# Kernel optimization log

Hardware: AMD Instinct MI355X
Metric: run time of the kernel (lower is better)

Reference implementation:

```python
import jax, jax.numpy as jnp
import numpy as np

WINDOW = 10
STRIDES = 1
EPS = 1e-5


def setup_inputs() -> dict:
    key = jax.random.key(0)
    B, T, F = 128, 512, 40
    tensors = jax.random.normal(key, (B, T, F), dtype=jnp.float32)
    return {"tensors": tensors}


def reference(tensors):
    # tensors: [B, T, F]
    B, T, F = tensors.shape
    # window start positions, replicating the module's iter_list logic
    starts = np.arange(0, T - WINDOW + 1, STRIDES)
    if (T - WINDOW) not in starts:
        starts = np.append(starts, T - WINDOW)
    # [S, W] gather indices -> windowed view [B, S, W, F]
    idx = starts[:, None] + np.arange(WINDOW)[None, :]
    xw = tensors[:, idx, :]  # [B, S, W, F]

    mean = xw.mean(axis=2)  # [B, S, F] == K.mean over window axis
    # K.std: population std (ddof=0) over the window axis
    std = jnp.sqrt(((xw - mean[:, :, None, :]) ** 2).mean(axis=2))  # [B, S, F]
    # K.switch(is_nan(std), mean-mean, std): NaN std -> 0
    std = jnp.where(jnp.isnan(std), jnp.zeros_like(std), std) + EPS

    # E[x_i * x_j] over window for all feature pairs: [B, S, F, F]
    Exy = jnp.einsum('bswi,bswj->bsij', xw, xw) / WINDOW
    cov = Exy - mean[:, :, :, None] * mean[:, :, None, :]
    corr = cov / (std[:, :, :, None] * std[:, :, None, :])  # [B, S, F, F]

    # itertools.combinations(range(F), 2) order == upper-triangular row-major
    iu, ju = np.triu_indices(F, 1)
    return corr[:, :, iu, ju]  # [B, S, C] with C = F*(F-1)/2
```

## Files before the change

### kernel.cpp

```cpp
#include <hip/hip_runtime.h>

#define BB   128
#define TT   512
#define FF   40
#define WW   10
#define NS   503
#define NP   780
#define SC   64
#define NCHUNK 8
#define ROWS (SC + WW - 1)
#define NSLOT 4
#define EPSC 1e-5f

__global__ __launch_bounds__(256, 4) void ts_corr_roll2(const float* __restrict__ in,
                                                        float* __restrict__ out) {
    const int blk = blockIdx.x;
    const int b   = blk / NCHUNK;
    const int c   = blk - b * NCHUNK;
    const int s0  = (c == NCHUNK - 1) ? (NS - SC) : c * SC;
    const int tid = threadIdx.x;

    __shared__ float  xs[ROWS][FF];
    __shared__ float2 st[SC][FF];

    const float4* src4 = (const float4*)(in + ((size_t)b * TT + s0) * FF);
    float4* xs4 = (float4*)&xs[0][0];
    #pragma unroll
    for (int k = 0; k < 3; ++k) {
        const int i = tid + k * 256;
        if (i < ROWS * FF / 4) xs4[i] = src4[i];
    }
    __syncthreads();

    #pragma unroll
    for (int k = 0; k < 10; ++k) {
        const int cell = tid + k * 256;
        const int t = cell / FF;
        const int f = cell - t * FF;
        float sx = 0.f, sxx = 0.f;
        #pragma unroll
        for (int w = 0; w < WW; ++w) {
            const float x = xs[t + w][f];
            sx += x; sxx += x * x;
        }
        const float m = sx * 0.1f;
        const float v = fmaxf(sxx * 0.1f - m * m, 0.f);
        const float istd = 1.0f / (sqrtf(v) + EPSC);
        st[t][f] = make_float2(istd, m * istd);
    }

    int  pi[NSLOT], pj[NSLOT];
    bool act[NSLOT];
    float sxy[NSLOT], ph[NSLOT][WW];
    #pragma unroll
    for (int k = 0; k < NSLOT; ++k) {
        const int p = tid + k * 256;
        act[k] = (p < NP);
        const int pp = act[k] ? p : 0;
        int i = (int)((79.0f - sqrtf((float)(6241 - 8 * pp))) * 0.5f);
        while (i > 0 && i * (79 - i) / 2 > pp) --i;
        while ((i + 1) * (79 - (i + 1)) / 2 <= pp) ++i;
        pi[k] = i;
        pj[k] = pp - i * (79 - i) / 2 + i + 1;
        float s = 0.f;
        #pragma unroll
        for (int w = 0; w < WW; ++w) {
            const float pr = xs[w][pi[k]] * xs[w][pj[k]];
            ph[k][w] = pr;
            s += pr;
        }
        sxy[k] = s;
    }
    __syncthreads();

    float* dst0 = out + (size_t)(b * NS + s0) * NP;
    for (int t0 = 0; t0 < SC; t0 += WW) {
        #pragma unroll
        for (int u = 0; u < WW; ++u) {
            const int t = t0 + u;
            if (t >= SC) break;
            float* dst = dst0 + (size_t)t * NP;
            #pragma unroll
            for (int k = 0; k < NSLOT; ++k) {
                if (!act[k]) continue;
                const float2 si = st[t][pi[k]];
                const float2 sj = st[t][pj[k]];
                dst[tid + k * 256] = sxy[k] * 0.1f * si.x * sj.x - si.y * sj.y;
                if (t + 1 < SC) {
                    const float pn = xs[t + WW][pi[k]] * xs[t + WW][pj[k]];
                    sxy[k] += pn - ph[k][u];
                    ph[k][u] = pn;
                }
            }
        }
    }
}

extern "C" void kernel_launch(void* const* d_in, const int* in_sizes, int n_in,
                              void* d_out, int out_size, void* d_ws, size_t ws_size,
                              hipStream_t stream) {
    const float* in = (const float*)d_in[0];
    float* out = (float*)d_out;
    ts_corr_roll2<<<BB * NCHUNK, 256, 0, stream>>>(in, out);
}
```

Measured before the change: 51.07 us.

## Map each thread to a strip of four adjacent pairs with vectorized LDS reads

Reassigns work so each of 210 threads handles one row and four consecutive column indices, loading neighbor features and stats as float4 from shared memory. Per-window stats are also computed four features at a time. This reduces LDS traffic and index math per pair, but global stores become strided per instruction and fewer threads are active.

```diff
diff --git a/kernel.cpp b/kernel.cpp
--- a/kernel.cpp
+++ b/kernel.cpp
@@ -9,10 +9,10 @@
 #define SC   64
 #define NCHUNK 8
 #define ROWS (SC + WW - 1)
-#define NSLOT 4
+#define NSTRIP 210
 #define EPSC 1e-5f
 
-__global__ __launch_bounds__(256, 4) void ts_corr_roll2(const float* __restrict__ in,
+__global__ __launch_bounds__(256, 4) void ts_corr_strip(const float* __restrict__ in,
                                                         float* __restrict__ out) {
     const int blk = blockIdx.x;
     const int b   = blk / NCHUNK;
@@ -27,70 +27,88 @@
     float4* xs4 = (float4*)&xs[0][0];
     #pragma unroll
     for (int k = 0; k < 3; ++k) {
-        const int i = tid + k * 256;
-        if (i < ROWS * FF / 4) xs4[i] = src4[i];
+        const int idx = tid + k * 256;
+        if (idx < ROWS * FF / 4) xs4[idx] = src4[idx];
     }
     __syncthreads();
 
     #pragma unroll
-    for (int k = 0; k < 10; ++k) {
-        const int cell = tid + k * 256;
-        const int t = cell / FF;
-        const int f = cell - t * FF;
-        float sx = 0.f, sxx = 0.f;
-        #pragma unroll
-        for (int w = 0; w < WW; ++w) {
-            const float x = xs[t + w][f];
-            sx += x; sxx += x * x;
+    for (int k = 0; k < 3; ++k) {
+        const int qd = tid + k * 256;
+        if (qd < SC * FF / 4) {
+            const int t  = qd / 10;
+            const int f0 = (qd - t * 10) * 4;
+            float sx0=0,sx1=0,sx2=0,sx3=0, sq0=0,sq1=0,sq2=0,sq3=0;
+            #pragma unroll
+            for (int w = 0; w < WW; ++w) {
+                const float4 x = *(const float4*)&xs[t + w][f0];
+                sx0 += x.x; sx1 += x.y; sx2 += x.z; sx3 += x.w;
+                sq0 += x.x*x.x; sq1 += x.y*x.y; sq2 += x.z*x.z; sq3 += x.w*x.w;
+            }
+            const float m0 = sx0*0.1f, m1 = sx1*0.1f, m2 = sx2*0.1f, m3 = sx3*0.1f;
+            const float u0 = 1.f/(sqrtf(fmaxf(sq0*0.1f - m0*m0, 0.f)) + EPSC);
+            const float u1 = 1.f/(sqrtf(fmaxf(sq1*0.1f - m1*m1, 0.f)) + EPSC);
+            const float u2 = 1.f/(sqrtf(fmaxf(sq2*0.1f - m2*m2, 0.f)) + EPSC);
+            const float u3 = 1.f/(sqrtf(fmaxf(sq3*0.1f - m3*m3, 0.f)) + EPSC);
+            *(float4*)&st[t][f0]     = make_float4(u0, m0*u0, u1, m1*u1);
+            *(float4*)&st[t][f0 + 2] = make_float4(u2, m2*u2, u3, m3*u3);
         }
-        const float m = sx * 0.1f;
-        const float v = fmaxf(sxx * 0.1f - m * m, 0.f);
-        const float istd = 1.0f / (sqrtf(v) + EPSC);
-        st[t][f] = make_float2(istd, m * istd);
     }
 
-    int  pi[NSLOT], pj[NSLOT];
-    bool act[NSLOT];
-    float sxy[NSLOT], ph[NSLOT][WW];
+    int row = 0, j0 = 0;
+    const bool sact = (tid < NSTRIP);
+    {
+        int rem = sact ? tid : 0;
+        for (int r = 0; r < FF; ++r) {
+            const int cnt = 10 - ((r + 1) >> 2);
+            if (rem < cnt) { row = r; j0 = (((r + 1) >> 2) + rem) << 2; break; }
+            rem -= cnt;
+        }
+    }
+    bool val[4];
     #pragma unroll
-    for (int k = 0; k < NSLOT; ++k) {
-        const int p = tid + k * 256;
-        act[k] = (p < NP);
-        const int pp = act[k] ? p : 0;
-        int i = (int)((79.0f - sqrtf((float)(6241 - 8 * pp))) * 0.5f);
-        while (i > 0 && i * (79 - i) / 2 > pp) --i;
-        while ((i + 1) * (79 - (i + 1)) / 2 <= pp) ++i;
-        pi[k] = i;
-        pj[k] = pp - i * (79 - i) / 2 + i + 1;
-        float s = 0.f;
-        #pragma unroll
-        for (int w = 0; w < WW; ++w) {
-            const float pr = xs[w][pi[k]] * xs[w][pj[k]];
-            ph[k][w] = pr;
-            s += pr;
-        }
-        sxy[k] = s;
+    for (int q = 0; q < 4; ++q) val[q] = sact && (j0 + q > row);
+    const int rowoff = row * (79 - row) / 2 - row - 1;
+
+    float sxy[4] = {0.f, 0.f, 0.f, 0.f};
+    float ph[4][WW];
+    #pragma unroll
+    for (int w = 0; w < WW; ++w) {
+        const float  xi = xs[w][row];
+        const float4 xj = *(const float4*)&xs[w][j0];
+        const float p0 = xi*xj.x, p1 = xi*xj.y, p2 = xi*xj.z, p3 = xi*xj.w;
+        ph[0][w] = p0; sxy[0] += p0;
+        ph[1][w] = p1; sxy[1] += p1;
+        ph[2][w] = p2; sxy[2] += p2;
+        ph[3][w] = p3; sxy[3] += p3;
     }
     __syncthreads();
 
-    float* dst0 = out + (size_t)(b * NS + s0) * NP;
+    if (!sact) return;
+
+    float* dst0 = out + (size_t)(b * NS + s0) * NP + rowoff;
     for (int t0 = 0; t0 < SC; t0 += WW) {
         #pragma unroll
         for (int u = 0; u < WW; ++u) {
             const int t = t0 + u;
-            if (t >= SC) break;
+            if (t0 == 60 && u >= 4) break;
+            const float2 sti = st[t][row];
+            const float4 a0  = *(const float4*)&st[t][j0];
+            const float4 a1  = *(const float4*)&st[t][j0 + 2];
+            const float  sui = sti.x * 0.1f;
             float* dst = dst0 + (size_t)t * NP;
-            #pragma unroll
-            for (int k = 0; k < NSLOT; ++k) {
-                if (!act[k]) continue;
-                const float2 si = st[t][pi[k]];
-                const float2 sj = st[t][pj[k]];
-                dst[tid + k * 256] = sxy[k] * 0.1f * si.x * sj.x - si.y * sj.y;
-                if (t + 1 < SC) {
-                    const float pn = xs[t + WW][pi[k]] * xs[t + WW][pj[k]];
-                    sxy[k] += pn - ph[k][u];
-                    ph[k][u] = pn;
-                }
+            if (val[0]) dst[j0]     = sxy[0] * sui * a0.x - sti.y * a0.y;
+            if (val[1]) dst[j0 + 1] = sxy[1] * sui * a0.z - sti.y * a0.w;
+            if (val[2]) dst[j0 + 2] = sxy[2] * sui * a1.x - sti.y * a1.y;
+            if (val[3]) dst[j0 + 3] = sxy[3] * sui * a1.z - sti.y * a1.w;
+            if (t + 1 < SC) {
+                const float  xi = xs[t + WW][row];
+                const float4 xj = *(const float4*)&xs[t + WW][j0];
+                float pn;
+                pn = xi*xj.x; sxy[0] += pn - ph[0][u]; ph[0][u] = pn;
+                pn = xi*xj.y; sxy[1] += pn - ph[1][u]; ph[1][u] = pn;
+                pn = xi*xj.z; sxy[2] += pn - ph[2][u]; ph[2][u] = pn;
+                pn = xi*xj.w; sxy[3] += pn - ph[3][u]; ph[3][u] = pn;
             }
         }
     }
@@ -101,5 +119,5 @@
                               hipStream_t stream) {
     const float* in = (const float*)d_in[0];
     float* out = (float*)d_out;
-    ts_corr_roll2<<<BB * NCHUNK, 256, 0, stream>>>(in, out);
+    ts_corr_strip<<<BB * NCHUNK, 256, 0, stream>>>(in, out);
 }
```

After: 110.9 us. 117% more time.

## Vectorize stats pass, fold 1/W into scale, and unroll output loop two rows at a time

Applied to the files above, without the earlier changes.

The per-window mean and inverse-std pass now handles four features per thread with float4 shared loads and stores. The 0.1 factor is folded into the stored scale as sqrt(0.1), which drops one multiply per output. The output loop is hand-unrolled by two time steps, with shared loads batched ahead and the rolling sum update interleaved between them. Per-slot active checks are replaced by a tid<12 branch for the fourth slot. All of this aims to cut LDS and ALU instruction count in the output-bound loop, at the cost of more registers and a hard-coded schedule.

```diff
diff --git a/kernel.cpp b/kernel.cpp
--- a/kernel.cpp
+++ b/kernel.cpp
@@ -9,18 +9,18 @@
 #define SC   64
 #define NCHUNK 8
 #define ROWS (SC + WW - 1)
-#define NSLOT 4
 #define EPSC 1e-5f
+#define C01  0.31622776601683794f
 
-__global__ __launch_bounds__(256, 4) void ts_corr_roll2(const float* __restrict__ in,
-                                                        float* __restrict__ out) {
+__global__ __launch_bounds__(256, 4) void ts_corr_r6(const float* __restrict__ in,
+                                                     float* __restrict__ out) {
     const int blk = blockIdx.x;
     const int b   = blk / NCHUNK;
     const int c   = blk - b * NCHUNK;
     const int s0  = (c == NCHUNK - 1) ? (NS - SC) : c * SC;
     const int tid = threadIdx.x;
 
-    __shared__ float  xs[ROWS][FF];
+    __shared__ float  xs[SC + WW][FF];
     __shared__ float2 st[SC][FF];
 
     const float4* src4 = (const float4*)(in + ((size_t)b * TT + s0) * FF);
@@ -33,30 +33,34 @@
     __syncthreads();
 
     #pragma unroll
-    for (int k = 0; k < 10; ++k) {
-        const int cell = tid + k * 256;
-        const int t = cell / FF;
-        const int f = cell - t * FF;
-        float sx = 0.f, sxx = 0.f;
-        #pragma unroll
-        for (int w = 0; w < WW; ++w) {
-            const float x = xs[t + w][f];
-            sx += x; sxx += x * x;
+    for (int k = 0; k < 3; ++k) {
+        const int qd = tid + k * 256;
+        if (qd < SC * FF / 4) {
+            const int t  = qd / 10;
+            const int f0 = (qd - t * 10) * 4;
+            float sx0=0,sx1=0,sx2=0,sx3=0, sq0=0,sq1=0,sq2=0,sq3=0;
+            #pragma unroll
+            for (int w = 0; w < WW; ++w) {
+                const float4 x = *(const float4*)&xs[t + w][f0];
+                sx0 += x.x; sx1 += x.y; sx2 += x.z; sx3 += x.w;
+                sq0 += x.x*x.x; sq1 += x.y*x.y; sq2 += x.z*x.z; sq3 += x.w*x.w;
+            }
+            const float m0 = sx0*0.1f, m1 = sx1*0.1f, m2 = sx2*0.1f, m3 = sx3*0.1f;
+            const float u0 = 1.f/(sqrtf(fmaxf(sq0*0.1f - m0*m0, 0.f)) + EPSC);
+            const float u1 = 1.f/(sqrtf(fmaxf(sq1*0.1f - m1*m1, 0.f)) + EPSC);
+            const float u2 = 1.f/(sqrtf(fmaxf(sq2*0.1f - m2*m2, 0.f)) + EPSC);
+            const float u3 = 1.f/(sqrtf(fmaxf(sq3*0.1f - m3*m3, 0.f)) + EPSC);
+            *(float4*)&st[t][f0]     = make_float4(u0*C01, m0*u0, u1*C01, m1*u1);
+            *(float4*)&st[t][f0 + 2] = make_float4(u2*C01, m2*u2, u3*C01, m3*u3);
         }
-        const float m = sx * 0.1f;
-        const float v = fmaxf(sxx * 0.1f - m * m, 0.f);
-        const float istd = 1.0f / (sqrtf(v) + EPSC);
-        st[t][f] = make_float2(istd, m * istd);
     }
 
-    int  pi[NSLOT], pj[NSLOT];
-    bool act[NSLOT];
-    float sxy[NSLOT], ph[NSLOT][WW];
+    int pi[4], pj[4];
+    float sxy[4], ph[4][WW];
     #pragma unroll
-    for (int k = 0; k < NSLOT; ++k) {
+    for (int k = 0; k < 4; ++k) {
         const int p = tid + k * 256;
-        act[k] = (p < NP);
-        const int pp = act[k] ? p : 0;
+        const int pp = (p < NP) ? p : 0;
         int i = (int)((79.0f - sqrtf((float)(6241 - 8 * pp))) * 0.5f);
         while (i > 0 && i * (79 - i) / 2 > pp) --i;
         while ((i + 1) * (79 - (i + 1)) / 2 <= pp) ++i;
@@ -73,27 +77,55 @@
     }
     __syncthreads();
 
-    float* dst0 = out + (size_t)(b * NS + s0) * NP;
-    for (int t0 = 0; t0 < SC; t0 += WW) {
-        #pragma unroll
-        for (int u = 0; u < WW; ++u) {
-            const int t = t0 + u;
-            if (t >= SC) break;
-            float* dst = dst0 + (size_t)t * NP;
-            #pragma unroll
-            for (int k = 0; k < NSLOT; ++k) {
-                if (!act[k]) continue;
-                const float2 si = st[t][pi[k]];
-                const float2 sj = st[t][pj[k]];
-                dst[tid + k * 256] = sxy[k] * 0.1f * si.x * sj.x - si.y * sj.y;
-                if (t + 1 < SC) {
-                    const float pn = xs[t + WW][pi[k]] * xs[t + WW][pj[k]];
-                    sxy[k] += pn - ph[k][u];
-                    ph[k][u] = pn;
-                }
-            }
-        }
+    float* dst0 = out + (size_t)(b * NS + s0) * NP + tid;
+
+#define STEP2(U, TA, DO2) do {                                                  \
+    const int _tA = (TA);                                                       \
+    float* _dA = dst0 + (size_t)_tA * NP;                                       \
+    float* _dB = _dA + NP;                                                      \
+    _Pragma("unroll")                                                           \
+    for (int k = 0; k < 3; ++k) {                                               \
+        const int _ii = pi[k], _jj = pj[k];                                     \
+        const float  _xiA = xs[_tA + WW][_ii], _xiB = xs[_tA + WW + 1][_ii];    \
+        const float  _xjA = xs[_tA + WW][_jj], _xjB = xs[_tA + WW + 1][_jj];    \
+        const float2 _siA = st[_tA][_ii],      _siB = st[_tA + 1][_ii];         \
+        const float2 _sjA = st[_tA][_jj],      _sjB = st[_tA + 1][_jj];         \
+        _dA[k * 256] = sxy[k] * _siA.x * _sjA.x - _siA.y * _sjA.y;              \
+        const float _pn = _xiA * _xjA;                                          \
+        sxy[k] += _pn - ph[k][U]; ph[k][U] = _pn;                               \
+        _dB[k * 256] = sxy[k] * _siB.x * _sjB.x - _siB.y * _sjB.y;              \
+        if (DO2) {                                                              \
+            const float _p2 = _xiB * _xjB;                                      \
+            sxy[k] += _p2 - ph[k][(U) + 1]; ph[k][(U) + 1] = _p2;               \
+        }                                                                       \
+    }                                                                           \
+    if (tid < 12) {                                                             \
+        const int _ii = pi[3], _jj = pj[3];                                     \
+        const float  _xiA = xs[_tA + WW][_ii], _xiB = xs[_tA + WW + 1][_ii];    \
+        const float  _xjA = xs[_tA + WW][_jj], _xjB = xs[_tA + WW + 1][_jj];    \
+        const float2 _siA = st[_tA][_ii],      _siB = st[_tA + 1][_ii];         \
+        const float2 _sjA = st[_tA][_jj],      _sjB = st[_tA + 1][_jj];         \
+        _dA[768] = sxy[3] * _siA.x * _sjA.x - _siA.y * _sjA.y;                  \
+        const float _pn = _xiA * _xjA;                                          \
+        sxy[3] += _pn - ph[3][U]; ph[3][U] = _pn;                               \
+        _dB[768] = sxy[3] * _siB.x * _sjB.x - _siB.y * _sjB.y;                  \
+        if (DO2) {                                                              \
+            const float _p2 = _xiB * _xjB;                                      \
+            sxy[3] += _p2 - ph[3][(U) + 1]; ph[3][(U) + 1] = _p2;               \
+        }                                                                       \
+    }                                                                           \
+} while (0)
+
+    for (int t0 = 0; t0 < 60; t0 += WW) {
+        STEP2(0, t0,     true);
+        STEP2(2, t0 + 2, true);
+        STEP2(4, t0 + 4, true);
+        STEP2(6, t0 + 6, true);
+        STEP2(8, t0 + 8, true);
     }
+    STEP2(0, 60, true);
+    STEP2(2, 62, false);
+#undef STEP2
 }
 
 extern "C" void kernel_launch(void* const* d_in, const int* in_sizes, int n_in,
@@ -101,5 +133,5 @@
                               hipStream_t stream) {
     const float* in = (const float*)d_in[0];
     float* out = (float*)d_out;
-    ts_corr_roll2<<<BB * NCHUNK, 256, 0, stream>>>(in, out);
+    ts_corr_r6<<<BB * NCHUNK, 256, 0, stream>>>(in, out);
 }
```

Result: faster. 47.34 us (-7.3%).

## Transpose shared tiles, store stats as half2, use 512 threads with vectorized rolling updates

Applied to the files above, without the earlier changes.

Stores the input window transposed (feature-major) in shared memory so each thread can read four consecutive time steps of its pair features with single float4 loads, and stores the per-time inverse std and scaled mean as packed half2 values read four at a time. The mean/std pass becomes a rolling sliding-window update per feature instead of recomputing each window. Blocks grow to 512 threads with two pair slots per thread, and the time loop is manually unrolled in steps of four. The aim is to cut LDS instruction count and per-thread overhead in the store-bound inner loop. Keeping the statistics in fp16 lowers correlation precision and may exceed tolerance.

```diff
diff --git a/kernel.cpp b/kernel.cpp
--- a/kernel.cpp
+++ b/kernel.cpp
@@ -1,4 +1,5 @@
 #include <hip/hip_runtime.h>
+#include <hip/hip_fp16.h>
 
 #define BB   128
 #define TT   512
@@ -8,55 +9,68 @@
 #define NP   780
 #define SC   64
 #define NCHUNK 8
-#define ROWS (SC + WW - 1)
-#define NSLOT 4
+#define NT   512
+#define XCOL 76
+#define SCOL 68
 #define EPSC 1e-5f
+#define C01  0.31622776601683794f
 
-__global__ __launch_bounds__(256, 4) void ts_corr_roll2(const float* __restrict__ in,
-                                                        float* __restrict__ out) {
+__global__ __launch_bounds__(NT) void ts_corr_r14(const float* __restrict__ in,
+                                                  float* __restrict__ out) {
     const int blk = blockIdx.x;
-    const int b   = blk / NCHUNK;
-    const int c   = blk - b * NCHUNK;
+    const int b   = blk >> 3;
+    const int c   = blk & (NCHUNK - 1);
     const int s0  = (c == NCHUNK - 1) ? (NS - SC) : c * SC;
     const int tid = threadIdx.x;
 
-    __shared__ float  xs[ROWS][FF];
-    __shared__ float2 st[SC][FF];
+    __shared__ __align__(16) float   xs_t[FF][XCOL];
+    __shared__ __align__(16) __half2 st_t[FF][SCOL];
 
     const float4* src4 = (const float4*)(in + ((size_t)b * TT + s0) * FF);
-    float4* xs4 = (float4*)&xs[0][0];
     #pragma unroll
-    for (int k = 0; k < 3; ++k) {
-        const int i = tid + k * 256;
-        if (i < ROWS * FF / 4) xs4[i] = src4[i];
+    for (int k = 0; k < 2; ++k) {
+        const int q = tid + k * NT;
+        if (q < (SC + WW - 1) * FF / 4) {
+            const int r  = q / 10;
+            const int f0 = (q - r * 10) * 4;
+            const float4 v = src4[q];
+            xs_t[f0    ][2 + r] = v.x;
+            xs_t[f0 + 1][2 + r] = v.y;
+            xs_t[f0 + 2][2 + r] = v.z;
+            xs_t[f0 + 3][2 + r] = v.w;
+        }
     }
     __syncthreads();
 
-    #pragma unroll
-    for (int k = 0; k < 10; ++k) {
-        const int cell = tid + k * 256;
-        const int t = cell / FF;
-        const int f = cell - t * FF;
-        float sx = 0.f, sxx = 0.f;
+    if (tid < 320) {
+        const int f  = tid >> 3;
+        const int t0 = (tid & 7) * 8;
+        float sx = 0.f, sq = 0.f;
         #pragma unroll
         for (int w = 0; w < WW; ++w) {
-            const float x = xs[t + w][f];
-            sx += x; sxx += x * x;
+            const float x = xs_t[f][2 + t0 + w];
+            sx += x; sq += x * x;
         }
-        const float m = sx * 0.1f;
-        const float v = fmaxf(sxx * 0.1f - m * m, 0.f);
-        const float istd = 1.0f / (sqrtf(v) + EPSC);
-        st[t][f] = make_float2(istd, m * istd);
+        #pragma unroll
+        for (int u = 0; u < 8; ++u) {
+            const int t = t0 + u;
+            const float m  = sx * 0.1f;
+            const float vv = fmaxf(sq * 0.1f - m * m, 0.f);
+            const float iu = 1.f / (sqrtf(vv) + EPSC);
+            st_t[f][t] = __floats2half2_rn(iu * C01, m * iu);
+            if (u < 7) {
+                const float xo = xs_t[f][2 + t], xn = xs_t[f][2 + t + WW];
+                sx += xn - xo; sq += xn * xn - xo * xo;
+            }
+        }
     }
 
-    int  pi[NSLOT], pj[NSLOT];
-    bool act[NSLOT];
-    float sxy[NSLOT], ph[NSLOT][WW];
+    int pi[2], pj[2];
+    float sxy[2], ph[2][WW];
     #pragma unroll
-    for (int k = 0; k < NSLOT; ++k) {
-        const int p = tid + k * 256;
-        act[k] = (p < NP);
-        const int pp = act[k] ? p : 0;
+    for (int k = 0; k < 2; ++k) {
+        const int p0 = tid + k * NT;
+        const int pp = (p0 < NP) ? p0 : 0;
         int i = (int)((79.0f - sqrtf((float)(6241 - 8 * pp))) * 0.5f);
         while (i > 0 && i * (79 - i) / 2 > pp) --i;
         while ((i + 1) * (79 - (i + 1)) / 2 <= pp) ++i;
@@ -64,36 +78,65 @@
         pj[k] = pp - i * (79 - i) / 2 + i + 1;
         float s = 0.f;
         #pragma unroll
-        for (int w = 0; w < WW; ++w) {
-            const float pr = xs[w][pi[k]] * xs[w][pj[k]];
-            ph[k][w] = pr;
-            s += pr;
+        for (int w2 = 0; w2 < WW; w2 += 2) {
+            const float2 a  = *(const float2*)&xs_t[pi[k]][2 + w2];
+            const float2 bb = *(const float2*)&xs_t[pj[k]][2 + w2];
+            const float q0 = a.x * bb.x, q1 = a.y * bb.y;
+            ph[k][w2] = q0; ph[k][w2 + 1] = q1;
+            s += q0 + q1;
         }
         sxy[k] = s;
     }
     __syncthreads();
 
-    float* dst0 = out + (size_t)(b * NS + s0) * NP;
-    for (int t0 = 0; t0 < SC; t0 += WW) {
-        #pragma unroll
-        for (int u = 0; u < WW; ++u) {
-            const int t = t0 + u;
-            if (t >= SC) break;
-            float* dst = dst0 + (size_t)t * NP;
-            #pragma unroll
-            for (int k = 0; k < NSLOT; ++k) {
-                if (!act[k]) continue;
-                const float2 si = st[t][pi[k]];
-                const float2 sj = st[t][pj[k]];
-                dst[tid + k * 256] = sxy[k] * 0.1f * si.x * sj.x - si.y * sj.y;
-                if (t + 1 < SC) {
-                    const float pn = xs[t + WW][pi[k]] * xs[t + WW][pj[k]];
-                    sxy[k] += pn - ph[k][u];
-                    ph[k][u] = pn;
-                }
-            }
-        }
+    const bool act1 = (tid < NP - NT);
+    float* dst0 = out + (size_t)(b * NS + s0) * NP + tid;
+
+#define H2F2(U) __half22float2(__builtin_bit_cast(__half2, (U)))
+
+#define SLOT4(K, OFF, U0, U1, U2, U3, DOLAST) do {                              \
+    const float4 _xi = *(const float4*)&xs_t[pi[K]][2 + _tA + WW];              \
+    const float4 _xj = *(const float4*)&xs_t[pj[K]][2 + _tA + WW];              \
+    const uint4  _si = *(const uint4*)&st_t[pi[K]][_tA];                        \
+    const uint4  _sj = *(const uint4*)&st_t[pj[K]][_tA];                        \
+    float2 _a, _b2; float _pn;                                                  \
+    _a = H2F2(_si.x); _b2 = H2F2(_sj.x);                                        \
+    _d0[OFF] = sxy[K] * _a.x * _b2.x - _a.y * _b2.y;                            \
+    _pn = _xi.x * _xj.x; sxy[K] += _pn - ph[K][U0]; ph[K][U0] = _pn;            \
+    _a = H2F2(_si.y); _b2 = H2F2(_sj.y);                                        \
+    _d1[OFF] = sxy[K] * _a.x * _b2.x - _a.y * _b2.y;                            \
+    _pn = _xi.y * _xj.y; sxy[K] += _pn - ph[K][U1]; ph[K][U1] = _pn;            \
+    _a = H2F2(_si.z); _b2 = H2F2(_sj.z);                                        \
+    _d2[OFF] = sxy[K] * _a.x * _b2.x - _a.y * _b2.y;                            \
+    _pn = _xi.z * _xj.z; sxy[K] += _pn - ph[K][U2]; ph[K][U2] = _pn;            \
+    _a = H2F2(_si.w); _b2 = H2F2(_sj.w);                                        \
+    _d3[OFF] = sxy[K] * _a.x * _b2.x - _a.y * _b2.y;                            \
+    if (DOLAST) {                                                               \
+        _pn = _xi.w * _xj.w; sxy[K] += _pn - ph[K][U3]; ph[K][U3] = _pn;        \
+    }                                                                           \
+} while (0)
+
+#define STEP4(U0, U1, U2, U3, TA, DOLAST) do {                                  \
+    const int _tA = (TA);                                                       \
+    float* _d0 = dst0 + (size_t)_tA * NP;                                       \
+    float* _d1 = _d0 + NP;                                                      \
+    float* _d2 = _d0 + 2 * NP;                                                  \
+    float* _d3 = _d0 + 3 * NP;                                                  \
+    SLOT4(0, 0, U0, U1, U2, U3, DOLAST);                                        \
+    if (act1) SLOT4(1, NT, U0, U1, U2, U3, DOLAST);                             \
+} while (0)
+
+    for (int t0 = 0; t0 < 60; t0 += 20) {
+        STEP4(0, 1, 2, 3, t0,      true);
+        STEP4(4, 5, 6, 7, t0 + 4,  true);
+        STEP4(8, 9, 0, 1, t0 + 8,  true);
+        STEP4(2, 3, 4, 5, t0 + 12, true);
+        STEP4(6, 7, 8, 9, t0 + 16, true);
     }
+    STEP4(0, 1, 2, 3, 60, false);
+#undef STEP4
+#undef SLOT4
+#undef H2F2
 }
 
 extern "C" void kernel_launch(void* const* d_in, const int* in_sizes, int n_in,
@@ -101,5 +144,5 @@
                               hipStream_t stream) {
     const float* in = (const float*)d_in[0];
     float* out = (float*)d_out;
-    ts_corr_roll2<<<BB * NCHUNK, 256, 0, stream>>>(in, out);
+    ts_corr_r14<<<BB * NCHUNK, NT, 0, stream>>>(in, out);
 }
```

New measurement: 44.02 us. 1.16x faster.
